# Kernel tuning notes

Hardware: AMD Instinct MI355X
Metric: run time of the kernel (lower is better)

## Reference

```python
import jax, jax.numpy as jnp
import numpy as np

B, S, D = 8, 2048, 1024  # batch, seq_len, embed_dim
EPS = 1e-12  # torch F.normalize default eps


def setup_inputs() -> dict:
    key = jax.random.key(0)
    ks = jax.random.split(key, 8)
    lin = 1.0 / np.sqrt(D)  # ~ torch Linear init scale
    return {
        "x": jax.random.normal(ks[0], (B, S, D), jnp.float32),
        "Wq": jax.random.uniform(ks[1], (D, D), jnp.float32, -lin, lin),
        "bq": jax.random.uniform(ks[2], (D,), jnp.float32, -lin, lin),
        "Wk": jax.random.uniform(ks[3], (D, D), jnp.float32, -lin, lin),
        "bk": jax.random.uniform(ks[4], (D,), jnp.float32, -lin, lin),
        "Wv": jax.random.uniform(ks[5], (D, D), jnp.float32, -lin, lin),
        "bv": jax.random.uniform(ks[6], (D,), jnp.float32, -lin, lin),
        # rotation params; module views the first S*S entries as an (S,S) matrix
        "rot": jax.random.normal(ks[7], (S * S,), jnp.float32),
    }


def _quantum_mask(rot):
    # F.normalize(mat, dim=-1) followed by elementwise square
    mat = rot[: S * S].reshape(S, S)
    nrm = jnp.sqrt(jnp.sum(mat * mat, axis=-1, keepdims=True))
    mat = mat / jnp.maximum(nrm, EPS)
    return mat * mat  # (S, S), rows sum to 1


def reference(x, Wq, bq, Wk, bk, Wv, bv, rot):
    # x: (B, S, D)
    q = x @ Wq.T + bq
    k = x @ Wk.T + bk
    v = x @ Wv.T + bv
    scale = 1.0 / np.sqrt(D)
    scores = jax.nn.softmax(jnp.einsum("bqd,bkd->bqk", q, k) * scale, axis=-1)
    hybrid = scores * _quantum_mask(rot)[None, :, :]  # broadcast over batch
    return jnp.einsum("bqk,bkd->bqd", hybrid, v)
```

## Files before the change

### kernel.cpp

```cpp
#include <hip/hip_runtime.h>

typedef unsigned short u16;
typedef u16 u16x4 __attribute__((ext_vector_type(4)));
typedef u16 u16x8 __attribute__((ext_vector_type(8)));
typedef __bf16 bf16x8 __attribute__((ext_vector_type(8)));
typedef float f32x4 __attribute__((ext_vector_type(4)));

#define GL2LDS(gp, lp)                                                          \
  __builtin_amdgcn_global_load_lds(                                             \
      (const __attribute__((address_space(1))) void*)(gp),                      \
      (__attribute__((address_space(3))) void*)(lp), 16, 0, 0)

__device__ __forceinline__ u16 f2bf(float f) {
  unsigned u = __builtin_bit_cast(unsigned, f);
  u += 0x7fffu + ((u >> 16) & 1u);
  return (u16)(u >> 16);
}

__device__ __forceinline__ float bf2f(u16 v) {
  unsigned u = ((unsigned)v) << 16;
  return __builtin_bit_cast(float, u);
}

__device__ __forceinline__ f32x4 mfma_bf16(u16x8 a, u16x8 b, f32x4 c) {
  return __builtin_amdgcn_mfma_f32_16x16x32_bf16(
      __builtin_bit_cast(bf16x8, a), __builtin_bit_cast(bf16x8, b), c, 0, 0, 0);
}

constexpr int BN_ = 8;
constexpr int S_ = 2048;
constexpr int D_ = 1024;

__global__ __launch_bounds__(256) void cvt_bf16(const float* __restrict__ in,
                                                u16* __restrict__ out, int n8) {
  int i = blockIdx.x * blockDim.x + threadIdx.x;
  int stride = gridDim.x * blockDim.x;
  for (; i < n8; i += stride) {
    const float4* p = reinterpret_cast<const float4*>(in) + (size_t)i * 2;
    float4 a = p[0], b = p[1];
    u16x8 o;
    o[0] = f2bf(a.x); o[1] = f2bf(a.y); o[2] = f2bf(a.z); o[3] = f2bf(a.w);
    o[4] = f2bf(b.x); o[5] = f2bf(b.y); o[6] = f2bf(b.z); o[7] = f2bf(b.w);
    reinterpret_cast<u16x8*>(out)[i] = o;
  }
}

__global__ __launch_bounds__(256) void concat3(const float* __restrict__ a,
                                               const float* __restrict__ b,
                                               const float* __restrict__ c,
                                               float* __restrict__ o) {
  int i = blockIdx.x * 256 + threadIdx.x;
  if (i < 1024) o[i] = a[i];
  else if (i < 2048) o[i] = b[i - 1024];
  else if (i < 3072) o[i] = c[i - 2048];
}

__global__ __launch_bounds__(256) void mask_kernel(const float* __restrict__ rot,
                                                   u16* __restrict__ msk,
                                                   float* __restrict__ rinv) {
  int r = blockIdx.x, t = threadIdx.x;
  const float4* p = reinterpret_cast<const float4*>(rot + (size_t)r * S_);
  float4 a = p[t], b = p[t + 256];
  float ax = a.x * a.x, ay = a.y * a.y, az = a.z * a.z, aw = a.w * a.w;
  float bx = b.x * b.x, by = b.y * b.y, bz = b.z * b.z, bw = b.w * b.w;
  u16x4 oa, ob;
  oa[0] = f2bf(ax); oa[1] = f2bf(ay); oa[2] = f2bf(az); oa[3] = f2bf(aw);
  ob[0] = f2bf(bx); ob[1] = f2bf(by); ob[2] = f2bf(bz); ob[3] = f2bf(bw);
  u16* mrow = msk + (size_t)r * S_;
  *reinterpret_cast<u16x4*>(mrow + t * 4) = oa;
  *reinterpret_cast<u16x4*>(mrow + 1024 + t * 4) = ob;
  float s = ax + ay + az + aw + bx + by + bz + bw;
#pragma unroll
  for (int d = 1; d < 64; d <<= 1) s += __shfl_xor(s, d);
  __shared__ float wsum[4];
  if ((t & 63) == 0) wsum[t >> 6] = s;
  __syncthreads();
  if (t == 0) {
    float ss = wsum[0] + wsum[1] + wsum[2] + wsum[3];
    rinv[r] = 1.0f / fmaxf(ss, 1e-24f);
  }
}

template <int NK>
__device__ __forceinline__ void kloop8(const u16* __restrict__ Abase,
                                       const u16* __restrict__ Bbase,
                                       int sA, int sB, u16* sh,
                                       f32x4 (&acc)[8][4]) {
  const int t = threadIdx.x;
  const int lane = t & 63, w = t >> 6;
  const int wm = w >> 2, wn = w & 3;
  const int lr = lane & 15;
  const int sl = (lane >> 4) ^ (((lr >> 3) & 1) << 1);
  const int aOff = (wm * 128 + lr) * 32 + sl * 8;
  const int bOff = 16384 + (wn * 64 + lr) * 32 + sl * 8;

  const int tr = t ^ (((t >> 5) & 1) << 1);
  const u16* aSrc = Abase + (size_t)(tr >> 2) * sA + (tr & 3) * 8;
  const u16* bSrc = Bbase + (size_t)(tr >> 2) * sB + (tr & 3) * 8;
  const size_t a128 = (size_t)128 * sA, b128 = (size_t)128 * sB;
  u16* dBase = sh + t * 8;

  auto stage = [&](int P, int op, int kk, int kt) {
    kt &= (NK - 1);
    const u16* s = (op ? bSrc : aSrc) + kt * 64 + kk * 32;
    u16* d = dBase + P * 32768 + op * 16384 + kk * 8192;
    GL2LDS(s, d);
    GL2LDS(s + (op ? b128 : a128), d + 4096);
  };

  u16x8 bf[4];

#define PHASE(P, kk, mh, sP, sOp, sKk, sKt, vm)                                  \
  do {                                                                           \
    const u16* ap_ = sh + (P) * 32768 + (kk) * 8192 + aOff;                      \
    u16x8 af_[4];                                                                \
    _Pragma("unroll")                                                            \
    for (int i_ = 0; i_ < 4; ++i_)                                               \
      af_[i_] = *reinterpret_cast<const u16x8*>(ap_ + ((mh) * 4 + i_) * 512);    \
    if ((mh) == 0) {                                                             \
      const u16* bp_ = sh + (P) * 32768 + (kk) * 8192 + bOff;                    \
      _Pragma("unroll")                                                          \
      for (int j_ = 0; j_ < 4; ++j_)                                             \
        bf[j_] = *reinterpret_cast<const u16x8*>(bp_ + j_ * 512);                \
    }                                                                            \
    stage(sP, sOp, sKk, sKt);                                                    \
    asm volatile("s_barrier" ::: "memory");                                      \
    __builtin_amdgcn_s_setprio(1);                                               \
    _Pragma("unroll")                                                            \
    for (int i_ = 0; i_ < 4; ++i_)                                               \
      _Pragma("unroll")                                                          \
      for (int j_ = 0; j_ < 4; ++j_)                                             \
        acc[(mh) * 4 + i_][j_] = mfma_bf16(af_[i_], bf[j_], acc[(mh) * 4 + i_][j_]); \
    __builtin_amdgcn_s_setprio(0);                                               \
    if (vm) asm volatile("s_waitcnt vmcnt(6)" ::: "memory");                     \
    asm volatile("s_barrier" ::: "memory");                                      \
  } while (0)

  stage(0, 1, 0, 0); stage(0, 0, 0, 0); stage(0, 1, 1, 0); stage(0, 0, 1, 0);
  stage(1, 1, 0, 1); stage(1, 0, 0, 1); stage(1, 1, 1, 1);
  asm volatile("s_waitcnt vmcnt(6)" ::: "memory");
  asm volatile("s_barrier" ::: "memory");

  for (int j2 = 0; j2 < NK / 2; ++j2) {
    const int kb = 2 * j2;
    PHASE(0, 0, 0, 1, 0, 1, kb + 1, false);
    PHASE(0, 0, 1, 0, 1, 0, kb + 2, false);
    PHASE(0, 1, 0, 0, 0, 0, kb + 2, false);
    PHASE(0, 1, 1, 0, 1, 1, kb + 2, true);
    PHASE(1, 0, 0, 0, 0, 1, kb + 2, false);
    PHASE(1, 0, 1, 1, 1, 0, kb + 3, false);
    PHASE(1, 1, 0, 1, 0, 0, kb + 3, false);
    PHASE(1, 1, 1, 1, 1, 1, kb + 3, true);
  }
#undef PHASE
}

__global__ __launch_bounds__(512, 2)
void gemm_qkv8(const u16* __restrict__ xb, const u16* __restrict__ wcat,
               const float* __restrict__ bcat, u16* __restrict__ qb,
               u16* __restrict__ kb, u16* __restrict__ vtb) {
  __shared__ alignas(16) u16 sh[65536];
  const int lin = blockIdx.x;
  const int swz = (lin & 7) * 96 + (lin >> 3);
  const int rt = swz / 12, ct = swz - rt * 12;
  const int rowBase = rt << 8, colBase = ct << 8;

  f32x4 acc[8][4] = {};
  kloop8<16>(xb + (size_t)rowBase * D_, wcat + (size_t)colBase * D_, D_, D_, sh, acc);

  const int t = threadIdx.x;
  const int lane = t & 63, w = t >> 6;
  const int wm = w >> 2, wn = w & 3;
  const int lrow4 = (lane >> 4) * 4, lcol = lane & 15;

  float bias[4];
#pragma unroll
  for (int j = 0; j < 4; ++j) bias[j] = bcat[colBase + wn * 64 + j * 16 + lcol];

  const int cls = colBase >> 10;
  const int ccol = colBase & 1023;
  if (cls < 2) {
    u16* out16 = (cls == 0) ? qb : kb;
#pragma unroll
    for (int i = 0; i < 8; ++i) {
#pragma unroll
      for (int jj = 0; jj < 4; ++jj) {
        int r = rowBase + wm * 128 + i * 16 + lrow4 + jj;
#pragma unroll
        for (int j = 0; j < 4; ++j) {
          int c = ccol + wn * 64 + j * 16 + lcol;
          out16[(size_t)r * D_ + c] = f2bf(acc[i][j][jj] + bias[j]);
        }
      }
    }
  } else {
    __syncthreads();
    u16 (*Ts)[136] = reinterpret_cast<u16(*)[136]>(sh);
    const int bq = rowBase >> 11, s0 = rowBase & (S_ - 1);
#pragma unroll
    for (int h = 0; h < 2; ++h) {
      if (wm == h) {
#pragma unroll
        for (int i = 0; i < 8; ++i)
#pragma unroll
          for (int jj = 0; jj < 4; ++jj)
#pragma unroll
            for (int j = 0; j < 4; ++j)
              Ts[wn * 64 + j * 16 + lcol][i * 16 + lrow4 + jj] =
                  f2bf(acc[i][j][jj] + bias[j]);
      }
      __syncthreads();
      const int col = t >> 1, ro = (t & 1) * 64;
      u16* dst = vtb + (size_t)bq * D_ * S_ + (size_t)(ccol + col) * S_ +
                 s0 + h * 128 + ro;
      const u16* srcp = &Ts[col][ro];
#pragma unroll
      for (int k2 = 0; k2 < 8; ++k2)
        *reinterpret_cast<u16x8*>(dst + k2 * 8) =
            *reinterpret_cast<const u16x8*>(srcp + k2 * 8);
      __syncthreads();
    }
  }
}

__global__ __launch_bounds__(512, 2)
void score8(const u16* __restrict__ qb, const u16* __restrict__ kb,
            const u16* __restrict__ msk, u16* __restrict__ hyb,
            float* __restrict__ Z) {
  __shared__ alignas(16) u16 sh[65536];
  const int lin = blockIdx.x;
  const int swz = (lin & 7) * 64 + (lin >> 3);
  const int b = swz >> 6, rt = (swz >> 3) & 7, ct = swz & 7;
  const int rowBase = rt << 8, colBase = ct << 8;

  f32x4 acc[8][4] = {};
  kloop8<16>(qb + ((size_t)(b * S_ + rowBase)) * D_,
             kb + ((size_t)(b * S_ + colBase)) * D_, D_, D_, sh, acc);

  const int t = threadIdx.x;
  const int lane = t & 63, w = t >> 6;
  const int wm = w >> 2, wn = w & 3;
  const int lrow4 = (lane >> 4) * 4, lcol = lane & 15;

#pragma unroll
  for (int i = 0; i < 8; ++i) {
    const int rowL = rowBase + wm * 128 + i * 16 + lrow4;
    f32x4 zrow = {0.f, 0.f, 0.f, 0.f};
#pragma unroll
    for (int j = 0; j < 4; ++j) {
      const int col = colBase + wn * 64 + j * 16 + lcol;
#pragma unroll
      for (int jj = 0; jj < 4; ++jj) {
        const int row = rowL + jj;
        float e = __expf(acc[i][j][jj] * 0.03125f);
        hyb[((size_t)(b * S_ + row)) * S_ + col] =
            f2bf(e * bf2f(msk[(size_t)row * S_ + col]));
        zrow[jj] += e;
      }
    }
#pragma unroll
    for (int d = 1; d < 16; d <<= 1) {
      zrow[0] += __shfl_xor(zrow[0], d);
      zrow[1] += __shfl_xor(zrow[1], d);
      zrow[2] += __shfl_xor(zrow[2], d);
      zrow[3] += __shfl_xor(zrow[3], d);
    }
    if (lcol == 0) {
#pragma unroll
      for (int jj = 0; jj < 4; ++jj)
        atomicAdd(&Z[b * S_ + rowL + jj], zrow[jj]);
    }
  }
}

__global__ __launch_bounds__(512, 2)
void gemm_pv8(const u16* __restrict__ hyb, const u16* __restrict__ vtb,
              const float* __restrict__ Z, const float* __restrict__ rinv,
              float* __restrict__ outp) {
  __shared__ alignas(16) u16 sh[65536];
  const int lin = blockIdx.x;
  const int swz = (lin & 7) * 32 + (lin >> 3);
  const int b = swz >> 5, rt = (swz >> 2) & 7, ct = swz & 3;
  const int rowBase = rt << 8, colBase = ct << 8;

  f32x4 acc[8][4] = {};
  kloop8<32>(hyb + (size_t)b * S_ * S_ + (size_t)rowBase * S_,
             vtb + (size_t)b * D_ * S_ + (size_t)colBase * S_, S_, S_, sh, acc);

  const int t = threadIdx.x;
  const int lane = t & 63, w = t >> 6;
  const int wm = w >> 2, wn = w & 3;
  const int lrow4 = (lane >> 4) * 4, lcol = lane & 15;

  float* outf = outp + (size_t)b * S_ * D_;
  const float* Zb = Z + (size_t)b * S_;
#pragma unroll
  for (int i = 0; i < 8; ++i) {
#pragma unroll
    for (int jj = 0; jj < 4; ++jj) {
      int r = rowBase + wm * 128 + i * 16 + lrow4 + jj;
      float rz = rinv[r] / Zb[r];
#pragma unroll
      for (int j = 0; j < 4; ++j) {
        int c = colBase + wn * 64 + j * 16 + lcol;
        outf[(size_t)r * D_ + c] = acc[i][j][jj] * rz;
      }
    }
  }
}

extern "C" void kernel_launch(void* const* d_in, const int* in_sizes, int n_in,
                              void* d_out, int out_size, void* d_ws, size_t ws_size,
                              hipStream_t stream) {
  const float* x = (const float*)d_in[0];
  const float* Wq = (const float*)d_in[1];
  const float* bq = (const float*)d_in[2];
  const float* Wk = (const float*)d_in[3];
  const float* bk = (const float*)d_in[4];
  const float* Wv = (const float*)d_in[5];
  const float* bv = (const float*)d_in[6];
  const float* rot = (const float*)d_in[7];

  char* ws = (char*)d_ws;
  size_t off = 0;
  auto take = [&](size_t bytes) {
    char* p = ws + off;
    off += (bytes + 255) & ~(size_t)255;
    return p;
  };
  u16* xb = (u16*)take((size_t)BN_ * S_ * D_ * 2);
  u16* wcat = (u16*)take((size_t)3 * D_ * D_ * 2);
  float* bcat = (float*)take((size_t)3 * D_ * 4);
  u16* qb = (u16*)take((size_t)BN_ * S_ * D_ * 2);
  u16* kbuf = (u16*)take((size_t)BN_ * S_ * D_ * 2);
  u16* vtb = (u16*)take((size_t)BN_ * S_ * D_ * 2);
  u16* hyb = (u16*)take((size_t)BN_ * S_ * S_ * 2);
  u16* msk = (u16*)take((size_t)S_ * S_ * 2);
  float* Zb = (float*)take((size_t)BN_ * S_ * 4);
  float* rinv = (float*)take((size_t)S_ * 4);

  (void)hipMemsetAsync(Zb, 0, (size_t)BN_ * S_ * 4, stream);

  cvt_bf16<<<2048, 256, 0, stream>>>(x, xb, BN_ * S_ * D_ / 8);
  cvt_bf16<<<512, 256, 0, stream>>>(Wq, wcat, D_ * D_ / 8);
  cvt_bf16<<<512, 256, 0, stream>>>(Wk, wcat + (size_t)D_ * D_, D_ * D_ / 8);
  cvt_bf16<<<512, 256, 0, stream>>>(Wv, wcat + (size_t)2 * D_ * D_, D_ * D_ / 8);
  concat3<<<12, 256, 0, stream>>>(bq, bk, bv, bcat);
  mask_kernel<<<S_, 256, 0, stream>>>(rot, msk, rinv);

  gemm_qkv8<<<768, 512, 0, stream>>>(xb, wcat, bcat, qb, kbuf, vtb);

  score8<<<512, 512, 0, stream>>>(qb, kbuf, msk, hyb, Zb);

  gemm_pv8<<<256, 512, 0, stream>>>(hyb, vtb, Zb, rinv, (float*)d_out);
}
```

Baseline: 301.9 us.

## Make QKV and score GEMMs persistent over column tiles, read rot directly

```diff
diff --git a/kernel.cpp b/kernel.cpp
--- a/kernel.cpp
+++ b/kernel.cpp
@@ -15,11 +15,6 @@
   unsigned u = __builtin_bit_cast(unsigned, f);
   u += 0x7fffu + ((u >> 16) & 1u);
   return (u16)(u >> 16);
-}
-
-__device__ __forceinline__ float bf2f(u16 v) {
-  unsigned u = ((unsigned)v) << 16;
-  return __builtin_bit_cast(float, u);
 }
 
 __device__ __forceinline__ f32x4 mfma_bf16(u16x8 a, u16x8 b, f32x4 c) {
@@ -55,21 +50,13 @@
   else if (i < 3072) o[i] = c[i - 2048];
 }
 
-__global__ __launch_bounds__(256) void mask_kernel(const float* __restrict__ rot,
-                                                   u16* __restrict__ msk,
+__global__ __launch_bounds__(256) void rinv_kernel(const float* __restrict__ rot,
                                                    float* __restrict__ rinv) {
   int r = blockIdx.x, t = threadIdx.x;
   const float4* p = reinterpret_cast<const float4*>(rot + (size_t)r * S_);
   float4 a = p[t], b = p[t + 256];
-  float ax = a.x * a.x, ay = a.y * a.y, az = a.z * a.z, aw = a.w * a.w;
-  float bx = b.x * b.x, by = b.y * b.y, bz = b.z * b.z, bw = b.w * b.w;
-  u16x4 oa, ob;
-  oa[0] = f2bf(ax); oa[1] = f2bf(ay); oa[2] = f2bf(az); oa[3] = f2bf(aw);
-  ob[0] = f2bf(bx); ob[1] = f2bf(by); ob[2] = f2bf(bz); ob[3] = f2bf(bw);
-  u16* mrow = msk + (size_t)r * S_;
-  *reinterpret_cast<u16x4*>(mrow + t * 4) = oa;
-  *reinterpret_cast<u16x4*>(mrow + 1024 + t * 4) = ob;
-  float s = ax + ay + az + aw + bx + by + bz + bw;
+  float s = a.x * a.x + a.y * a.y + a.z * a.z + a.w * a.w +
+            b.x * b.x + b.y * b.y + b.z * b.z + b.w * b.w;
 #pragma unroll
   for (int d = 1; d < 64; d <<= 1) s += __shfl_xor(s, d);
   __shared__ float wsum[4];
@@ -81,7 +68,34 @@
   }
 }
 
-template <int NK>
+__device__ __forceinline__ void stage_one(const u16* aSrc, const u16* bSrc,
+                                          size_t a128, size_t b128, u16* dBase,
+                                          int P, int op, int kk, int kt, int NK) {
+  if (kt >= NK) return;
+  const u16* s = (op ? bSrc : aSrc) + kt * 64 + kk * 32;
+  u16* d = dBase + P * 32768 + op * 16384 + kk * 8192;
+  GL2LDS(s, d);
+  GL2LDS(s + (op ? b128 : a128), d + 4096);
+}
+
+__device__ __forceinline__ void pro7(const u16* Abase, const u16* Bbase,
+                                     int sA, int sB, u16* sh) {
+  const int t = threadIdx.x;
+  const int tr = t ^ (((t >> 5) & 1) << 1);
+  const u16* aSrc = Abase + (size_t)(tr >> 2) * sA + (tr & 3) * 8;
+  const u16* bSrc = Bbase + (size_t)(tr >> 2) * sB + (tr & 3) * 8;
+  const size_t a128 = (size_t)128 * sA, b128 = (size_t)128 * sB;
+  u16* dBase = sh + t * 8;
+  stage_one(aSrc, bSrc, a128, b128, dBase, 0, 1, 0, 0, 99);
+  stage_one(aSrc, bSrc, a128, b128, dBase, 0, 0, 0, 0, 99);
+  stage_one(aSrc, bSrc, a128, b128, dBase, 0, 1, 1, 0, 99);
+  stage_one(aSrc, bSrc, a128, b128, dBase, 0, 0, 1, 0, 99);
+  stage_one(aSrc, bSrc, a128, b128, dBase, 1, 1, 0, 1, 99);
+  stage_one(aSrc, bSrc, a128, b128, dBase, 1, 0, 0, 1, 99);
+  stage_one(aSrc, bSrc, a128, b128, dBase, 1, 1, 1, 1, 99);
+}
+
+template <int NK, bool PRO>
 __device__ __forceinline__ void kloop8(const u16* __restrict__ Abase,
                                        const u16* __restrict__ Bbase,
                                        int sA, int sB, u16* sh,
@@ -99,14 +113,6 @@
   const u16* bSrc = Bbase + (size_t)(tr >> 2) * sB + (tr & 3) * 8;
   const size_t a128 = (size_t)128 * sA, b128 = (size_t)128 * sB;
   u16* dBase = sh + t * 8;
-
-  auto stage = [&](int P, int op, int kk, int kt) {
-    kt &= (NK - 1);
-    const u16* s = (op ? bSrc : aSrc) + kt * 64 + kk * 32;
-    u16* d = dBase + P * 32768 + op * 16384 + kk * 8192;
-    GL2LDS(s, d);
-    GL2LDS(s + (op ? b128 : a128), d + 4096);
-  };
 
   u16x8 bf[4];
 
@@ -123,7 +129,7 @@
       for (int j_ = 0; j_ < 4; ++j_)                                             \
         bf[j_] = *reinterpret_cast<const u16x8*>(bp_ + j_ * 512);                \
     }                                                                            \
-    stage(sP, sOp, sKk, sKt);                                                    \
+    stage_one(aSrc, bSrc, a128, b128, dBase, sP, sOp, sKk, sKt, NK);             \
     asm volatile("s_barrier" ::: "memory");                                      \
     __builtin_amdgcn_s_setprio(1);                                               \
     _Pragma("unroll")                                                            \
@@ -136,22 +142,23 @@
     asm volatile("s_barrier" ::: "memory");                                      \
   } while (0)
 
-  stage(0, 1, 0, 0); stage(0, 0, 0, 0); stage(0, 1, 1, 0); stage(0, 0, 1, 0);
-  stage(1, 1, 0, 1); stage(1, 0, 0, 1); stage(1, 1, 1, 1);
-  asm volatile("s_waitcnt vmcnt(6)" ::: "memory");
+  if (PRO) pro7(Abase, Bbase, sA, sB, sh);
+  asm volatile("s_waitcnt vmcnt(3)" ::: "memory");
   asm volatile("s_barrier" ::: "memory");
 
   for (int j2 = 0; j2 < NK / 2; ++j2) {
     const int kb = 2 * j2;
-    PHASE(0, 0, 0, 1, 0, 1, kb + 1, false);
-    PHASE(0, 0, 1, 0, 1, 0, kb + 2, false);
-    PHASE(0, 1, 0, 0, 0, 0, kb + 2, false);
-    PHASE(0, 1, 1, 0, 1, 1, kb + 2, true);
-    PHASE(1, 0, 0, 0, 0, 1, kb + 2, false);
-    PHASE(1, 0, 1, 1, 1, 0, kb + 3, false);
-    PHASE(1, 1, 0, 1, 0, 0, kb + 3, false);
-    PHASE(1, 1, 1, 1, 1, 1, kb + 3, true);
-  }
+    const int kt1 = kb + 1, kt2 = kb + 2, kt3 = kb + 3;
+    PHASE(0, 0, 0, 1, 0, 1, kt1, false);
+    PHASE(0, 0, 1, 0, 1, 0, kt2, false);
+    PHASE(0, 1, 0, 0, 0, 0, kt2, false);
+    PHASE(0, 1, 1, 0, 1, 1, kt2, true);
+    PHASE(1, 0, 0, 0, 0, 1, kt2, false);
+    PHASE(1, 0, 1, 1, 1, 0, kt3, false);
+    PHASE(1, 1, 0, 1, 0, 0, kt3, false);
+    PHASE(1, 1, 1, 1, 1, 1, kt3, true);
+  }
+  asm volatile("s_waitcnt vmcnt(0)" ::: "memory");
 #undef PHASE
 }
 
@@ -160,115 +167,132 @@
                const float* __restrict__ bcat, u16* __restrict__ qb,
                u16* __restrict__ kb, u16* __restrict__ vtb) {
   __shared__ alignas(16) u16 sh[65536];
-  const int lin = blockIdx.x;
-  const int swz = (lin & 7) * 96 + (lin >> 3);
-  const int rt = swz / 12, ct = swz - rt * 12;
-  const int rowBase = rt << 8, colBase = ct << 8;
-
-  f32x4 acc[8][4] = {};
-  kloop8<16>(xb + (size_t)rowBase * D_, wcat + (size_t)colBase * D_, D_, D_, sh, acc);
+  const int s = blockIdx.x;
+  const int xcd = s & 7, idx = s >> 3;
+  const int cg = xcd & 3;
+  const int rt = (xcd >> 2) * 32 + idx;
+  const int rowBase = rt << 8;
+  const u16* Abase = xb + (size_t)rowBase * D_;
 
   const int t = threadIdx.x;
   const int lane = t & 63, w = t >> 6;
   const int wm = w >> 2, wn = w & 3;
   const int lrow4 = (lane >> 4) * 4, lcol = lane & 15;
-
-  float bias[4];
-#pragma unroll
-  for (int j = 0; j < 4; ++j) bias[j] = bcat[colBase + wn * 64 + j * 16 + lcol];
-
-  const int cls = colBase >> 10;
-  const int ccol = colBase & 1023;
-  if (cls < 2) {
-    u16* out16 = (cls == 0) ? qb : kb;
-#pragma unroll
-    for (int i = 0; i < 8; ++i) {
-#pragma unroll
-      for (int jj = 0; jj < 4; ++jj) {
-        int r = rowBase + wm * 128 + i * 16 + lrow4 + jj;
-#pragma unroll
-        for (int j = 0; j < 4; ++j) {
-          int c = ccol + wn * 64 + j * 16 + lcol;
-          out16[(size_t)r * D_ + c] = f2bf(acc[i][j][jj] + bias[j]);
+  const int ccol = cg << 8;
+
+  for (int tile = 0; tile < 3; ++tile) {
+    const int colBase = (cg + tile * 4) << 8;
+    const u16* Bbase = wcat + (size_t)colBase * D_;
+    f32x4 acc[8][4] = {};
+    if (tile == 0) kloop8<16, true>(Abase, Bbase, D_, D_, sh, acc);
+    else           kloop8<16, false>(Abase, Bbase, D_, D_, sh, acc);
+    if (tile < 2)
+      pro7(Abase, wcat + (size_t)((cg + (tile + 1) * 4) << 8) * D_, D_, D_, sh);
+
+    float bias[4];
+#pragma unroll
+    for (int j = 0; j < 4; ++j) bias[j] = bcat[colBase + wn * 64 + j * 16 + lcol];
+
+    if (tile < 2) {
+      u16* out16 = (tile == 0) ? qb : kb;
+#pragma unroll
+      for (int i = 0; i < 8; ++i) {
+#pragma unroll
+        for (int jj = 0; jj < 4; ++jj) {
+          int r = rowBase + wm * 128 + i * 16 + lrow4 + jj;
+#pragma unroll
+          for (int j = 0; j < 4; ++j) {
+            int c = ccol + wn * 64 + j * 16 + lcol;
+            out16[(size_t)r * D_ + c] = f2bf(acc[i][j][jj] + bias[j]);
+          }
         }
       }
-    }
-  } else {
-    __syncthreads();
-    u16 (*Ts)[136] = reinterpret_cast<u16(*)[136]>(sh);
-    const int bq = rowBase >> 11, s0 = rowBase & (S_ - 1);
-#pragma unroll
-    for (int h = 0; h < 2; ++h) {
-      if (wm == h) {
-#pragma unroll
-        for (int i = 0; i < 8; ++i)
-#pragma unroll
-          for (int jj = 0; jj < 4; ++jj)
-#pragma unroll
-            for (int j = 0; j < 4; ++j)
-              Ts[wn * 64 + j * 16 + lcol][i * 16 + lrow4 + jj] =
-                  f2bf(acc[i][j][jj] + bias[j]);
-      }
-      __syncthreads();
-      const int col = t >> 1, ro = (t & 1) * 64;
-      u16* dst = vtb + (size_t)bq * D_ * S_ + (size_t)(ccol + col) * S_ +
-                 s0 + h * 128 + ro;
-      const u16* srcp = &Ts[col][ro];
-#pragma unroll
-      for (int k2 = 0; k2 < 8; ++k2)
-        *reinterpret_cast<u16x8*>(dst + k2 * 8) =
-            *reinterpret_cast<const u16x8*>(srcp + k2 * 8);
-      __syncthreads();
+    } else {
+      u16 (*Ts)[136] = reinterpret_cast<u16(*)[136]>(sh);
+      const int bq = rowBase >> 11, s0 = rowBase & (S_ - 1);
+#pragma unroll
+      for (int h = 0; h < 2; ++h) {
+        if (wm == h) {
+#pragma unroll
+          for (int i = 0; i < 8; ++i)
+#pragma unroll
+            for (int jj = 0; jj < 4; ++jj)
+#pragma unroll
+              for (int j = 0; j < 4; ++j)
+                Ts[wn * 64 + j * 16 + lcol][i * 16 + lrow4 + jj] =
+                    f2bf(acc[i][j][jj] + bias[j]);
+        }
+        __syncthreads();
+        const int col = t >> 1, ro = (t & 1) * 64;
+        u16* dst = vtb + (size_t)bq * D_ * S_ + (size_t)(ccol + col) * S_ +
+                   s0 + h * 128 + ro;
+        const u16* srcp = &Ts[col][ro];
+#pragma unroll
+        for (int k2 = 0; k2 < 8; ++k2)
+          *reinterpret_cast<u16x8*>(dst + k2 * 8) =
+              *reinterpret_cast<const u16x8*>(srcp + k2 * 8);
+        __syncthreads();
+      }
     }
   }
 }
 
 __global__ __launch_bounds__(512, 2)
 void score8(const u16* __restrict__ qb, const u16* __restrict__ kb,
-            const u16* __restrict__ msk, u16* __restrict__ hyb,
+            const float* __restrict__ rot, u16* __restrict__ hyb,
             float* __restrict__ Z) {
   __shared__ alignas(16) u16 sh[65536];
-  const int lin = blockIdx.x;
-  const int swz = (lin & 7) * 64 + (lin >> 3);
-  const int b = swz >> 6, rt = (swz >> 3) & 7, ct = swz & 7;
-  const int rowBase = rt << 8, colBase = ct << 8;
-
-  f32x4 acc[8][4] = {};
-  kloop8<16>(qb + ((size_t)(b * S_ + rowBase)) * D_,
-             kb + ((size_t)(b * S_ + colBase)) * D_, D_, D_, sh, acc);
+  const int s = blockIdx.x;
+  const int b = s & 7, idx = s >> 3;
+  const int rt = idx >> 2, cg = idx & 3;
+  const int rowBase = rt << 8;
+  const u16* Abase = qb + ((size_t)(b * S_ + rowBase)) * D_;
 
   const int t = threadIdx.x;
   const int lane = t & 63, w = t >> 6;
   const int wm = w >> 2, wn = w & 3;
   const int lrow4 = (lane >> 4) * 4, lcol = lane & 15;
 
+  float zacc[8][4] = {};
+
+  for (int tile = 0; tile < 2; ++tile) {
+    const int colBase = (cg + tile * 4) << 8;
+    const u16* Bbase = kb + ((size_t)(b * S_ + colBase)) * D_;
+    f32x4 acc[8][4] = {};
+    if (tile == 0) kloop8<16, true>(Abase, Bbase, D_, D_, sh, acc);
+    else           kloop8<16, false>(Abase, Bbase, D_, D_, sh, acc);
+    if (tile == 0)
+      pro7(Abase, kb + ((size_t)(b * S_ + ((cg + 4) << 8))) * D_, D_, D_, sh);
+
+#pragma unroll
+    for (int i = 0; i < 8; ++i) {
+      const int rowL = rowBase + wm * 128 + i * 16 + lrow4;
+#pragma unroll
+      for (int j = 0; j < 4; ++j) {
+        const int col = colBase + wn * 64 + j * 16 + lcol;
+#pragma unroll
+        for (int jj = 0; jj < 4; ++jj) {
+          const int row = rowL + jj;
+          float e = __expf(acc[i][j][jj] * 0.03125f);
+          float rv = rot[(size_t)row * S_ + col];
+          hyb[((size_t)(b * S_ + row)) * S_ + col] = f2bf(e * rv * rv);
+          zacc[i][jj] += e;
+        }
+      }
+    }
+  }
+
 #pragma unroll
   for (int i = 0; i < 8; ++i) {
-    const int rowL = rowBase + wm * 128 + i * 16 + lrow4;
-    f32x4 zrow = {0.f, 0.f, 0.f, 0.f};
-#pragma unroll
-    for (int j = 0; j < 4; ++j) {
-      const int col = colBase + wn * 64 + j * 16 + lcol;
-#pragma unroll
-      for (int jj = 0; jj < 4; ++jj) {
-        const int row = rowL + jj;
-        float e = __expf(acc[i][j][jj] * 0.03125f);
-        hyb[((size_t)(b * S_ + row)) * S_ + col] =
-            f2bf(e * bf2f(msk[(size_t)row * S_ + col]));
-        zrow[jj] += e;
-      }
-    }
-#pragma unroll
-    for (int d = 1; d < 16; d <<= 1) {
-      zrow[0] += __shfl_xor(zrow[0], d);
-      zrow[1] += __shfl_xor(zrow[1], d);
-      zrow[2] += __shfl_xor(zrow[2], d);
-      zrow[3] += __shfl_xor(zrow[3], d);
-    }
-    if (lcol == 0) {
-#pragma unroll
-      for (int jj = 0; jj < 4; ++jj)
-        atomicAdd(&Z[b * S_ + rowL + jj], zrow[jj]);
+#pragma unroll
+    for (int jj = 0; jj < 4; ++jj) {
+      float v = zacc[i][jj];
+#pragma unroll
+      for (int d = 1; d < 16; d <<= 1) v += __shfl_xor(v, d);
+      if (lcol == 0) {
+        int row = rowBase + wm * 128 + i * 16 + lrow4 + jj;
+        atomicAdd(&Z[b * S_ + row], v);
+      }
     }
   }
 }
@@ -284,8 +308,8 @@
   const int rowBase = rt << 8, colBase = ct << 8;
 
   f32x4 acc[8][4] = {};
-  kloop8<32>(hyb + (size_t)b * S_ * S_ + (size_t)rowBase * S_,
-             vtb + (size_t)b * D_ * S_ + (size_t)colBase * S_, S_, S_, sh, acc);
+  kloop8<32, true>(hyb + (size_t)b * S_ * S_ + (size_t)rowBase * S_,
+                   vtb + (size_t)b * D_ * S_ + (size_t)colBase * S_, S_, S_, sh, acc);
 
   const int t = threadIdx.x;
   const int lane = t & 63, w = t >> 6;
@@ -335,7 +359,6 @@
   u16* kbuf = (u16*)take((size_t)BN_ * S_ * D_ * 2);
   u16* vtb = (u16*)take((size_t)BN_ * S_ * D_ * 2);
   u16* hyb = (u16*)take((size_t)BN_ * S_ * S_ * 2);
-  u16* msk = (u16*)take((size_t)S_ * S_ * 2);
   float* Zb = (float*)take((size_t)BN_ * S_ * 4);
   float* rinv = (float*)take((size_t)S_ * 4);
 
@@ -346,11 +369,11 @@
   cvt_bf16<<<512, 256, 0, stream>>>(Wk, wcat + (size_t)D_ * D_, D_ * D_ / 8);
   cvt_bf16<<<512, 256, 0, stream>>>(Wv, wcat + (size_t)2 * D_ * D_, D_ * D_ / 8);
   concat3<<<12, 256, 0, stream>>>(bq, bk, bv, bcat);
-  mask_kernel<<<S_, 256, 0, stream>>>(rot, msk, rinv);
-
-  gemm_qkv8<<<768, 512, 0, stream>>>(xb, wcat, bcat, qb, kbuf, vtb);
-
-  score8<<<512, 512, 0, stream>>>(qb, kbuf, msk, hyb, Zb);
+  rinv_kernel<<<S_, 256, 0, stream>>>(rot, rinv);
+
+  gemm_qkv8<<<256, 512, 0, stream>>>(xb, wcat, bcat, qb, kbuf, vtb);
+
+  score8<<<256, 512, 0, stream>>>(qb, kbuf, rot, hyb, Zb);
 
   gemm_pv8<<<256, 512, 0, stream>>>(hyb, vtb, Zb, rinv, (float*)d_out);
 }
```

Result: slower. 374.3 us (+24.0%).

## Stage GEMM epilogues through LDS for coalesced 16-byte global stores

Applied to the files above, without the earlier changes.

```diff
diff --git a/kernel.cpp b/kernel.cpp
--- a/kernel.cpp
+++ b/kernel.cpp
@@ -30,6 +30,7 @@
 constexpr int BN_ = 8;
 constexpr int S_ = 2048;
 constexpr int D_ = 1024;
+constexpr int EP = 272;
 
 __global__ __launch_bounds__(256) void cvt_bf16(const float* __restrict__ in,
                                                 u16* __restrict__ out, int n8) {
@@ -180,18 +181,30 @@
   const int cls = colBase >> 10;
   const int ccol = colBase & 1023;
   if (cls < 2) {
+    __syncthreads();
     u16* out16 = (cls == 0) ? qb : kb;
 #pragma unroll
-    for (int i = 0; i < 8; ++i) {
-#pragma unroll
-      for (int jj = 0; jj < 4; ++jj) {
-        int r = rowBase + wm * 128 + i * 16 + lrow4 + jj;
-#pragma unroll
-        for (int j = 0; j < 4; ++j) {
-          int c = ccol + wn * 64 + j * 16 + lcol;
-          out16[(size_t)r * D_ + c] = f2bf(acc[i][j][jj] + bias[j]);
-        }
+    for (int h = 0; h < 2; ++h) {
+      if (wm == h) {
+#pragma unroll
+        for (int i = 0; i < 8; ++i)
+#pragma unroll
+          for (int jj = 0; jj < 4; ++jj) {
+            int rloc = i * 16 + lrow4 + jj;
+#pragma unroll
+            for (int j = 0; j < 4; ++j)
+              sh[rloc * EP + wn * 64 + j * 16 + lcol] = f2bf(acc[i][j][jj] + bias[j]);
+          }
       }
+      __syncthreads();
+#pragma unroll
+      for (int r2 = 0; r2 < 8; ++r2) {
+        int row = r2 * 16 + (t >> 5), chunk = t & 31;
+        u16x8 v = *reinterpret_cast<const u16x8*>(sh + row * EP + chunk * 8);
+        *reinterpret_cast<u16x8*>(out16 + (size_t)(rowBase + h * 128 + row) * D_ +
+                                  ccol + chunk * 8) = v;
+      }
+      __syncthreads();
     }
   } else {
     __syncthreads();
@@ -242,33 +255,51 @@
   const int wm = w >> 2, wn = w & 3;
   const int lrow4 = (lane >> 4) * 4, lcol = lane & 15;
 
+  float zacc[8][4] = {};
+
+  __syncthreads();
+#pragma unroll
+  for (int h = 0; h < 2; ++h) {
+    if (wm == h) {
+#pragma unroll
+      for (int i = 0; i < 8; ++i)
+#pragma unroll
+        for (int jj = 0; jj < 4; ++jj) {
+          const int rloc = i * 16 + lrow4 + jj;
+          const size_t mrow = (size_t)(rowBase + h * 128 + rloc) * S_;
+#pragma unroll
+          for (int j = 0; j < 4; ++j) {
+            const int cloc = wn * 64 + j * 16 + lcol;
+            float e = __expf(acc[i][j][jj] * 0.03125f);
+            zacc[i][jj] += e;
+            sh[rloc * EP + cloc] = f2bf(e * bf2f(msk[mrow + colBase + cloc]));
+          }
+        }
+    }
+    __syncthreads();
+#pragma unroll
+    for (int r2 = 0; r2 < 8; ++r2) {
+      int row = r2 * 16 + (t >> 5), chunk = t & 31;
+      u16x8 v = *reinterpret_cast<const u16x8*>(sh + row * EP + chunk * 8);
+      __builtin_nontemporal_store(
+          v, reinterpret_cast<u16x8*>(hyb +
+                                      ((size_t)(b * S_ + rowBase + h * 128 + row)) * S_ +
+                                      colBase + chunk * 8));
+    }
+    __syncthreads();
+  }
+
 #pragma unroll
   for (int i = 0; i < 8; ++i) {
-    const int rowL = rowBase + wm * 128 + i * 16 + lrow4;
-    f32x4 zrow = {0.f, 0.f, 0.f, 0.f};
-#pragma unroll
-    for (int j = 0; j < 4; ++j) {
-      const int col = colBase + wn * 64 + j * 16 + lcol;
-#pragma unroll
-      for (int jj = 0; jj < 4; ++jj) {
-        const int row = rowL + jj;
-        float e = __expf(acc[i][j][jj] * 0.03125f);
-        hyb[((size_t)(b * S_ + row)) * S_ + col] =
-            f2bf(e * bf2f(msk[(size_t)row * S_ + col]));
-        zrow[jj] += e;
+#pragma unroll
+    for (int jj = 0; jj < 4; ++jj) {
+      float v = zacc[i][jj];
+#pragma unroll
+      for (int d = 1; d < 16; d <<= 1) v += __shfl_xor(v, d);
+      if (lcol == 0) {
+        int row = rowBase + wm * 128 + i * 16 + lrow4 + jj;
+        atomicAdd(&Z[b * S_ + row], v);
       }
-    }
-#pragma unroll
-    for (int d = 1; d < 16; d <<= 1) {
-      zrow[0] += __shfl_xor(zrow[0], d);
-      zrow[1] += __shfl_xor(zrow[1], d);
-      zrow[2] += __shfl_xor(zrow[2], d);
-      zrow[3] += __shfl_xor(zrow[3], d);
-    }
-    if (lcol == 0) {
-#pragma unroll
-      for (int jj = 0; jj < 4; ++jj)
-        atomicAdd(&Z[b * S_ + rowL + jj], zrow[jj]);
     }
   }
 }
@@ -294,18 +325,36 @@
 
   float* outf = outp + (size_t)b * S_ * D_;
   const float* Zb = Z + (size_t)b * S_;
-#pragma unroll
-  for (int i = 0; i < 8; ++i) {
-#pragma unroll
-    for (int jj = 0; jj < 4; ++jj) {
-      int r = rowBase + wm * 128 + i * 16 + lrow4 + jj;
-      float rz = rinv[r] / Zb[r];
-#pragma unroll
-      for (int j = 0; j < 4; ++j) {
-        int c = colBase + wn * 64 + j * 16 + lcol;
-        outf[(size_t)r * D_ + c] = acc[i][j][jj] * rz;
+  float* Tf = reinterpret_cast<float*>(sh);
+
+  __syncthreads();
+#pragma unroll
+  for (int q = 0; q < 4; ++q) {
+    if (wm == (q >> 1)) {
+#pragma unroll
+      for (int i2 = 0; i2 < 4; ++i2) {
+        const int i = (q & 1) * 4 + i2;
+#pragma unroll
+        for (int jj = 0; jj < 4; ++jj) {
+          const int rl = i2 * 16 + lrow4 + jj;
+          const int r = rowBase + q * 64 + rl;
+          const float rz = rinv[r] / Zb[r];
+#pragma unroll
+          for (int j = 0; j < 4; ++j)
+            Tf[rl * EP + wn * 64 + j * 16 + lcol] = acc[i][j][jj] * rz;
+        }
       }
     }
+    __syncthreads();
+#pragma unroll
+    for (int r2 = 0; r2 < 8; ++r2) {
+      int rl = r2 * 8 + (t >> 6), chunk = t & 63;
+      f32x4 v = *reinterpret_cast<const f32x4*>(Tf + rl * EP + chunk * 4);
+      __builtin_nontemporal_store(
+          v, reinterpret_cast<f32x4*>(outf + (size_t)(rowBase + q * 64 + rl) * D_ +
+                                      colBase + chunk * 4));
+    }
+    __syncthreads();
   }
 }
 
```

Measured after the change: 316.0 us. 4.7% more time.
